# Optimization experiments

Hardware: AMD Instinct MI355X
Metric: run time of the kernel (lower is better)

Reference implementation:

```python
import jax, jax.numpy as jnp
import numpy as np

B, V, DIM, HEADS = 8192, 17, 192, 3
DKH = DIM // HEADS


def setup_inputs() -> dict:
    key = jax.random.key(0)
    ks = jax.random.split(key, 10)
    s = DIM ** -0.5
    return {
        "x": jax.random.normal(ks[0], (B, V, DIM), jnp.float32),
        "mask": jax.random.uniform(ks[1], (V, V), jnp.float32),
        "group_mask": jax.random.normal(ks[2], (B, HEADS, V, V), jnp.float32),
        "drop_mask": jax.random.bernoulli(ks[3], 0.5, (B, HEADS, V)).astype(jnp.float32),
        "qkv_w": jax.random.normal(ks[4], (3 * DIM, DIM), jnp.float32) * s,  # 1x1 conv == linear
        "qkv_b": jnp.zeros((3 * DIM,), jnp.float32),
        "attn_w": jax.random.normal(ks[5], (DIM, DIM), jnp.float32) * s,
        "attn_b": jnp.zeros((DIM,), jnp.float32),
        "key_rel": jax.random.normal(ks[6], (V * V - V, DKH), jnp.float32),
        "key_rel_diag": jax.random.normal(ks[7], (1, DKH), jnp.float32),
        "PA": jnp.ones((V, V), jnp.float32),
        "nn1_w": jax.random.normal(ks[8], (DIM, DIM), jnp.float32) * s,
        "nn1_b": jnp.zeros((DIM,), jnp.float32),
    }


def _forward(x, mask, group_mask, drop_mask, qkv_w, qkv_b, attn_w, attn_b,
             key_rel, key_rel_diag, PA, nn1_w, nn1_b):
    Bsz, Vn, C = x.shape
    Nh = HEADS
    dkh = C // Nh
    # 1x1 qkv conv over the channel axis (T=1 singleton time axis drops out)
    qkv = x @ qkv_w.T + qkv_b                      # (B, V, 3C)
    q, k, v = qkv[..., :C], qkv[..., C:2 * C], qkv[..., 2 * C:]

    def heads(t):
        return t.reshape(Bsz, Vn, Nh, dkh).transpose(0, 2, 1, 3)  # (B, Nh, V, dkh)

    q = heads(q) * (dkh ** -0.5)
    k = heads(k)
    v = heads(v)

    logits = jnp.einsum('bhid,bhjd->bhij', q, k)   # (B, Nh, V, V)
    logits = logits + (mask * PA)[None, None] + group_mask

    # relative position logits (rel_to_abs gather trick)
    rel = jnp.einsum('bhid,ijd->bhij', q, key_rel.reshape(Vn, Vn - 1, dkh))  # (B,Nh,V,V-1)
    diag = jnp.einsum('bhid,d->bhi', q, key_rel_diag[0])                     # (B,Nh,V)
    r = rel.reshape(Bsz, Nh, Vn - 1, Vn)           # reinterpret flat (V*(V-1)) as (V-1, V)
    r = jnp.concatenate([r, jnp.zeros((Bsz, Nh, 1, Vn), r.dtype)], axis=2)   # pad row -> (B,Nh,V,V)
    r = jnp.concatenate([diag[..., None], r], axis=3)                        # diag col -> (B,Nh,V,V+1)
    rel_logits = r.reshape(Bsz, Nh, Vn + 1, Vn)[:, :, :Vn, :]                # (B,Nh,V,V)

    w = jax.nn.softmax(logits + rel_logits, axis=-1)
    # stochastic column (key) mask + renormalize
    w = w * drop_mask[:, :, None, :]
    w = w / (w.sum(-1, keepdims=True) + 1e-8)

    out = jnp.einsum('bhij,bhjd->bhid', w, v)      # (B, Nh, V, dkh)
    out = out.transpose(0, 2, 1, 3).reshape(Bsz, Vn, C)  # combine heads (channel = h*dkh+d)
    out = out @ attn_w.T + attn_b                  # 1x1 attn_out conv
    out = out @ nn1_w.T + nn1_b                    # nn1 linear (dropout in eval -> identity)
    return out


def reference(x, mask, group_mask, drop_mask, qkv_w, qkv_b, attn_w, attn_b,
              key_rel, key_rel_diag, PA, nn1_w, nn1_b):
    return _forward(x, mask, group_mask, drop_mask, qkv_w, qkv_b, attn_w, attn_b,
                    key_rel, key_rel_diag, PA, nn1_w, nn1_b)
```

## Files before the change

kernel.cpp:

```cpp
#include <hip/hip_runtime.h>

typedef __attribute__((ext_vector_type(8))) short short8;
typedef __attribute__((ext_vector_type(4))) float f32x4;
typedef __attribute__((ext_vector_type(16))) float f32x16;
typedef unsigned short u16;
typedef unsigned int u32;

#define NB_TOT 8192
#define DIM 192

#define WN_OFF    0
#define WCN_OFF   221184
#define BC_OFF    294912
#define KRELF_OFF 295680
#define MPA_OFF   365312

#define XS_O  0
#define SF2_U16 3468
#define K_O   6944
#define V_O   13472
#define Q_O   22688
#define SMEM_U16 29264

__device__ __forceinline__ u16 f2b(float f) {
  u32 u = __float_as_uint(f);
  u32 r = u + 0x7FFFu + ((u >> 16) & 1u);
  return (u16)(r >> 16);
}

__device__ __forceinline__ int swzqk(int I) {
  return ((I & 7) << 3) ^ ((I & 8) << 1);
}

__device__ __forceinline__ void bar_lgkm() {
  asm volatile("s_waitcnt lgkmcnt(0)" ::: "memory");
  __builtin_amdgcn_s_barrier();
  asm volatile("" ::: "memory");
}

__global__ void prep_kernel(const float* __restrict__ qkv_w,
                            const float* __restrict__ attn_w,
                            const float* __restrict__ attn_b,
                            const float* __restrict__ nn1_w,
                            const float* __restrict__ nn1_b,
                            const float* __restrict__ key_rel,
                            const float* __restrict__ krd,
                            const float* __restrict__ mask,
                            const float* __restrict__ PA,
                            char* __restrict__ ws) {
  u16* wN    = (u16*)(ws + WN_OFF);
  u16* wcN   = (u16*)(ws + WCN_OFF);
  float* bc  = (float*)(ws + BC_OFF);
  u16* krelf = (u16*)(ws + KRELF_OFF);
  float* mpa = (float*)(ws + MPA_OFF);
  for (int idx = blockIdx.x * 256 + threadIdx.x; idx < 152289; idx += gridDim.x * 256) {
    if (idx < 110592) {
      wN[idx] = f2b(qkv_w[idx]);
    } else if (idx < 147456) {
      int t2 = idx - 110592; int n = t2 / 192, k = t2 - n * 192;
      float a = 0.f;
      for (int t = 0; t < 192; ++t) a = fmaf(nn1_w[n * 192 + t], attn_w[t * 192 + k], a);
      wcN[n * 192 + k] = f2b(a);
    } else if (idx < 147648) {
      int n = idx - 147456; float a = nn1_b[n];
      for (int t = 0; t < 192; ++t) a = fmaf(nn1_w[n * 192 + t], attn_b[t], a);
      bc[n] = a;
    } else if (idx < 152000) {
      int t = idx - 147648;
      int lane = t & 63, ks = (t >> 6) & 3, I = t >> 8;
      int J = lane & 31;
      int d0 = ks * 16 + (lane >> 5) * 8;
      u16 vals[8];
#pragma unroll
      for (int i = 0; i < 8; ++i) {
        float v = 0.f;
        if (J <= 16) {
          if (J == I) v = krd[d0 + i];
          else { int tt = 17 * I + J; int p = tt - tt / 18 - 1; v = key_rel[p * 64 + d0 + i]; }
        }
        vals[i] = f2b(v);
      }
      u32 w0 = vals[0] | ((u32)vals[1] << 16), w1 = vals[2] | ((u32)vals[3] << 16);
      u32 w2 = vals[4] | ((u32)vals[5] << 16), w3 = vals[6] | ((u32)vals[7] << 16);
      uint4 pk; pk.x = w0; pk.y = w1; pk.z = w2; pk.w = w3;
      *(uint4*)(krelf + (size_t)t * 8) = pk;
    } else {
      int i = idx - 152000; mpa[i] = mask[i] * PA[i];
    }
  }
}

__global__ __launch_bounds__(512, 4)
void fused_kernel(const float* __restrict__ x, const float* __restrict__ gm,
                  const float* __restrict__ drop, const float* __restrict__ qkv_b,
                  const u16* __restrict__ wN, const u16* __restrict__ wcN,
                  const float* __restrict__ bc, const u16* __restrict__ krelf,
                  const float* __restrict__ mpa, float* __restrict__ out) {
  __shared__ u16 smem[SMEM_U16];
  float* const Sf    = (float*)(smem + XS_O);
  float* const Sf2   = (float*)(smem + SF2_U16);
  u16*   const wbf   = smem + K_O;
  float* const dropl = (float*)(smem + K_O + 4080);

  const int tid = threadIdx.x;
  const int blk = blockIdx.x;
  const int lane = tid & 63;
  const int l31 = lane & 31;
  const int lh = lane >> 5;
  const int wv = tid >> 6;

  float drv = 0.f;
  if (tid < 102) drv = drop[(size_t)blk * 102 + tid];
  float gmr5[5] = {0.f, 0.f, 0.f, 0.f, 0.f};
  if (tid < 408) {
    int r = tid >> 2, sub = tid & 3;
    int bh = r / 17, I = r - bh * 17;
    const float* gmrow = gm + (size_t)blk * 1734 + bh * 289 + I * 17;
#pragma unroll
    for (int i = 0; i < 5; ++i) {
      int J = sub + 4 * i;
      if (J < 17) gmr5[i] = gmrow[J];
    }
  }

  const float* xb = x + (size_t)blk * 34 * 192;
  for (int idx = tid; idx < 1632; idx += 512) {
    int row = idx / 48, k4 = (idx - row * 48) * 4;
    float4 v = *(const float4*)(xb + row * 192 + k4);
    u16 p[4] = {f2b(v.x), f2b(v.y), f2b(v.z), f2b(v.w)};
    *(uint2*)(smem + XS_O + row * 200 + k4) = *(uint2*)p;
  }
  bar_lgkm();

  const int lrow = tid & 15, lg = (tid >> 4) & 3, kgrp = lg * 8;

  for (int Np = wv; Np < 18; Np += 8) {
    const int c0 = Np * 32;
    const int which = c0 / 192;
    const int hd0 = c0 - which * 192;
    const int h0 = hd0 >> 6,          h1 = (hd0 + 16) >> 6;
    const int d0 = (hd0 & 63) + lrow, d1 = ((hd0 + 16) & 63) + lrow;
    const u16* wB0 = wN + (size_t)(c0 + lrow) * 192;
    const u16* wB1 = wB0 + 16 * 192;
    short8 bfr0[6], bfr1[6];
#pragma unroll
    for (int kk = 0; kk < 6; ++kk) {
      bfr0[kk] = *(const short8*)(wB0 + kk * 32 + kgrp);
      bfr1[kk] = *(const short8*)(wB1 + kk * 32 + kgrp);
    }
    const float bias0 = qkv_b[c0 + lrow], bias1 = qkv_b[c0 + 16 + lrow];
    const float scale = which ? 1.0f : 0.125f;
#pragma unroll
    for (int m = 0; m < 3; ++m) {
      f32x4 acc0 = {}, acc1 = {};
#pragma unroll
      for (int kk = 0; kk < 6; ++kk) {
        short8 a = *(const short8*)(smem + XS_O + (m * 16 + lrow) * 200 + kk * 32 + kgrp);
        acc0 = __builtin_amdgcn_mfma_f32_16x16x32_bf16(a, bfr0[kk], acc0, 0, 0, 0);
        acc1 = __builtin_amdgcn_mfma_f32_16x16x32_bf16(a, bfr1[kk], acc1, 0, 0, 0);
      }
#pragma unroll
      for (int j = 0; j < 4; ++j) {
        int r = m * 16 + lg * 4 + j;
        if (r < 34) {
          int bi = r >= 17 ? 1 : 0, I = r - bi * 17;
          int slot = bi * 3 + h0, slot1 = bi * 3 + h1;
          u16 v0 = f2b((acc0[j] + bias0) * scale);
          u16 v1 = f2b((acc1[j] + bias1) * scale);
          if (which == 0) {
            smem[Q_O + slot  * 1096 + I * 64 + (d0 ^ swzqk(I))] = v0;
            smem[Q_O + slot1 * 1096 + I * 64 + (d1 ^ swzqk(I))] = v1;
          } else if (which == 1) {
            smem[K_O + slot  * 1088 + I * 64 + (d0 ^ swzqk(I))] = v0;
            smem[K_O + slot1 * 1088 + I * 64 + (d1 ^ swzqk(I))] = v1;
          } else {
            smem[V_O + slot  * 1536 + d0 * 24 + I] = v0;
            smem[V_O + slot1 * 1536 + d1 * 24 + I] = v1;
          }
        }
      }
    }
  }
  bar_lgkm();

  const int rowc = l31 < 16 ? l31 : 16;

  if (wv < 6) {
    int bh = wv;
    const u16* qb = smem + Q_O + bh * 1096;
    const u16* kb = smem + K_O + bh * 1088;
    const int swr = swzqk(rowc);
    f32x16 acc = {};
#pragma unroll
    for (int ks = 0; ks < 4; ++ks) {
      int off = (ks * 16 + lh * 8) ^ swr;
      short8 afr = *(const short8*)(qb + rowc * 64 + off);
      short8 bfr = *(const short8*)(kb + rowc * 64 + off);
      acc = __builtin_amdgcn_mfma_f32_32x32x16_bf16(afr, bfr, acc, 0, 0, 0);
    }
    if (l31 < 17) {
      float* Sb = Sf + bh * 289 + l31;
#pragma unroll
      for (int g = 0; g < 16; ++g) {
        int I = (g & 3) + 8 * (g >> 2) + 4 * lh;
        if (I < 17) Sb[I * 17] = acc[g];
      }
    }
  }
  for (int I = wv; I < 17; I += 8) {
    int bhA = l31 < 6 ? l31 : 5;
    const u16* qb = smem + Q_O + bhA * 1096 + I * 64;
    const int swz = swzqk(I);
    float mpav = (l31 < 17) ? mpa[I * 17 + l31] : 0.f;
    f32x16 acc = {};
#pragma unroll
    for (int ks = 0; ks < 4; ++ks) {
      short8 afr = *(const short8*)(qb + ((ks * 16 + lh * 8) ^ swz));
      short8 bfr = *(const short8*)(krelf + ((size_t)(I * 4 + ks) * 64 + lane) * 8);
      acc = __builtin_amdgcn_mfma_f32_32x32x16_bf16(afr, bfr, acc, 0, 0, 0);
    }
    if (l31 < 17) {
#pragma unroll
      for (int g = 0; g < 16; ++g) {
        int bh = (g & 3) + 8 * (g >> 2) + 4 * lh;
        if (bh < 6) Sf2[bh * 289 + I * 17 + l31] = acc[g] + mpav;
      }
    }
  }
  if (tid < 102) dropl[tid] = drv;
  bar_lgkm();

  if (tid < 408) {
    int r = tid >> 2, sub = tid & 3;
    int bh = r / 17, I = r - bh * 17;
    const float* Srow  = Sf  + bh * 289 + I * 17;
    const float* S2row = Sf2 + bh * 289 + I * 17;
    float lv[5];
    float mx = -3.4e38f;
#pragma unroll
    for (int i = 0; i < 5; ++i) {
      int J = sub + 4 * i;
      float v = -3.4e38f;
      if (J < 17) v = Srow[J] + S2row[J] + gmr5[i];
      lv[i] = v;
      mx = fmaxf(mx, v);
    }
    mx = fmaxf(mx, __shfl_xor(mx, 1, 4));
    mx = fmaxf(mx, __shfl_xor(mx, 2, 4));
    float s1 = 0.f;
#pragma unroll
    for (int i = 0; i < 5; ++i) {
      int J = sub + 4 * i;
      float e = 0.f;
      if (J < 17) e = __expf(lv[i] - mx);
      lv[i] = e; s1 += e;
    }
    s1 += __shfl_xor(s1, 1, 4);
    s1 += __shfl_xor(s1, 2, 4);
    float inv1 = 1.0f / s1, s2 = 0.f;
#pragma unroll
    for (int i = 0; i < 5; ++i) {
      int J = sub + 4 * i;
      float w2 = 0.f;
      if (J < 17) w2 = lv[i] * inv1 * dropl[bh * 17 + J];
      lv[i] = w2; s2 += w2;
    }
    s2 += __shfl_xor(s2, 1, 4);
    s2 += __shfl_xor(s2, 2, 4);
    float inv2 = 1.0f / (s2 + 1e-8f);
    u16* wr = wbf + r * 40;
    int swz = (I & 3) << 3;
#pragma unroll
    for (int i = 0; i < 8; ++i) {
      int J = sub + 4 * i;
      u16 val = 0;
      if (J < 17) val = f2b(lv[i] * inv2);
      wr[J ^ swz] = val;
    }
  }
  bar_lgkm();

  if (wv < 6) {
    int bh = wv;
    const u16* wb = wbf + (bh * 17 + rowc) * 40;
    int sw = (rowc & 3) << 3;
    short8 wa0 = *(const short8*)(wb + ((lh * 8) ^ sw));
    short8 wa1 = *(const short8*)(wb + ((lh * 8 + 16) ^ sw));
    int bi = bh >= 3 ? 1 : 0, h = bh - bi * 3;
    const u16* vb = smem + V_O + bh * 1536;
#pragma unroll
    for (int nt = 0; nt < 2; ++nt) {
      int d = nt * 32 + l31;
      short8 v0 = *(const short8*)(vb + d * 24 + lh * 8);
      f32x16 acc = {};
      acc = __builtin_amdgcn_mfma_f32_32x32x16_bf16(wa0, v0, acc, 0, 0, 0);
      short8 v1 = {};
      if (lh == 0) v1[0] = (short)vb[d * 24 + 16];
      acc = __builtin_amdgcn_mfma_f32_32x32x16_bf16(wa1, v1, acc, 0, 0, 0);
#pragma unroll
      for (int g = 0; g < 16; ++g) {
        int I = (g & 3) + 8 * (g >> 2) + 4 * lh;
        if (I < 17) smem[XS_O + (bi * 17 + I) * 200 + h * 64 + d] = f2b(acc[g]);
      }
    }
  }
  bar_lgkm();

  float* outb = out + (size_t)blk * 34 * 192;
  if (wv < 6) {
    const int nc0 = wv * 32 + lrow, nc1 = nc0 + 16;
    short8 bfr0[6], bfr1[6];
#pragma unroll
    for (int kk = 0; kk < 6; ++kk) {
      bfr0[kk] = *(const short8*)(wcN + (size_t)nc0 * 192 + kk * 32 + kgrp);
      bfr1[kk] = *(const short8*)(wcN + (size_t)nc1 * 192 + kk * 32 + kgrp);
    }
    const float bias0 = bc[nc0], bias1 = bc[nc1];
#pragma unroll
    for (int m = 0; m < 3; ++m) {
      f32x4 acc0 = {}, acc1 = {};
#pragma unroll
      for (int kk = 0; kk < 6; ++kk) {
        short8 a = *(const short8*)(smem + XS_O + (m * 16 + lrow) * 200 + kk * 32 + kgrp);
        acc0 = __builtin_amdgcn_mfma_f32_16x16x32_bf16(a, bfr0[kk], acc0, 0, 0, 0);
        acc1 = __builtin_amdgcn_mfma_f32_16x16x32_bf16(a, bfr1[kk], acc1, 0, 0, 0);
      }
#pragma unroll
      for (int j = 0; j < 4; ++j) {
        int r = m * 16 + lg * 4 + j;
        if (r < 34) {
          outb[(size_t)r * 192 + nc0] = acc0[j] + bias0;
          outb[(size_t)r * 192 + nc1] = acc1[j] + bias1;
        }
      }
    }
  }
}

extern "C" void kernel_launch(void* const* d_in, const int* in_sizes, int n_in,
                              void* d_out, int out_size, void* d_ws, size_t ws_size,
                              hipStream_t stream) {
  const float* x    = (const float*)d_in[0];
  const float* mask = (const float*)d_in[1];
  const float* gm   = (const float*)d_in[2];
  const float* drop = (const float*)d_in[3];
  const float* qkvw = (const float*)d_in[4];
  const float* qkvb = (const float*)d_in[5];
  const float* attw = (const float*)d_in[6];
  const float* attb = (const float*)d_in[7];
  const float* krel = (const float*)d_in[8];
  const float* krd  = (const float*)d_in[9];
  const float* PA   = (const float*)d_in[10];
  const float* nn1w = (const float*)d_in[11];
  const float* nn1b = (const float*)d_in[12];
  char* ws = (char*)d_ws;
  float* out = (float*)d_out;

  prep_kernel<<<600, 256, 0, stream>>>(qkvw, attw, attb, nn1w, nn1b, krel, krd, mask, PA, ws);

  const u16* wN    = (const u16*)(ws + WN_OFF);
  const u16* wcN   = (const u16*)(ws + WCN_OFF);
  const float* bc  = (const float*)(ws + BC_OFF);
  const u16* krelf = (const u16*)(ws + KRELF_OFF);
  const float* mpa = (const float*)(ws + MPA_OFF);

  fused_kernel<<<NB_TOT / 2, 512, 0, stream>>>(x, gm, drop, qkvb, wN, wcN, bc, krelf, mpa, out);
}
```

Measured before the change: 191.1 us.

## Split fused kernel into separate QKV GEMM and per-batch attention kernels

Adds a qkv_kernel that projects 64 rows of x at a time into a bf16 QKV buffer in the workspace, with the Q scale and bias already applied. It also adds an attn_kernel that runs one batch per 256-thread block, reads that buffer and performs attention plus the combined output projection. The aim is a larger, more efficient M-tile for the QKV GEMM and lower per-block shared memory, which should allow higher occupancy. The cost is an extra round trip through global memory for the roughly 160 MB bf16 QKV intermediate plus a second launch. The old fused kernel stays as a fallback when the workspace is too small.

```diff
diff --git a/kernel.cpp b/kernel.cpp
--- a/kernel.cpp
+++ b/kernel.cpp
@@ -14,13 +14,7 @@
 #define BC_OFF    294912
 #define KRELF_OFF 295680
 #define MPA_OFF   365312
-
-#define XS_O  0
-#define SF2_U16 3468
-#define K_O   6944
-#define V_O   13472
-#define Q_O   22688
-#define SMEM_U16 29264
+#define QKV_OFF   524288
 
 __device__ __forceinline__ u16 f2b(float f) {
   u32 u = __float_as_uint(f);
@@ -91,6 +85,265 @@
 }
 
 __global__ __launch_bounds__(512, 4)
+void qkv_kernel(const float* __restrict__ x, const u16* __restrict__ wN,
+                const float* __restrict__ qkv_b, u16* __restrict__ qkvo) {
+  __shared__ u16 xs[64 * 200];
+  const int tid = threadIdx.x;
+  const size_t R0 = (size_t)blockIdx.x * 64;
+  const float* xb = x + R0 * 192;
+  for (int idx = tid; idx < 3072; idx += 512) {
+    int row = idx / 48, k4 = (idx - row * 48) * 4;
+    float4 v = *(const float4*)(xb + row * 192 + k4);
+    u16 p[4] = {f2b(v.x), f2b(v.y), f2b(v.z), f2b(v.w)};
+    *(uint2*)(xs + row * 200 + k4) = *(uint2*)p;
+  }
+  bar_lgkm();
+  const int lrow = tid & 15, lg = (tid >> 4) & 3, kgrp = lg * 8;
+  const int wv = tid >> 6;
+  for (int Np = wv; Np < 18; Np += 8) {
+    const int c0 = Np * 32;
+    const int which = c0 / 192;
+    const u16* wB0 = wN + (size_t)(c0 + lrow) * 192;
+    const u16* wB1 = wB0 + 16 * 192;
+    short8 bfr0[6], bfr1[6];
+#pragma unroll
+    for (int kk = 0; kk < 6; ++kk) {
+      bfr0[kk] = *(const short8*)(wB0 + kk * 32 + kgrp);
+      bfr1[kk] = *(const short8*)(wB1 + kk * 32 + kgrp);
+    }
+    const float scale = which ? 1.0f : 0.125f;
+    const float bias0 = qkv_b[c0 + lrow], bias1 = qkv_b[c0 + 16 + lrow];
+#pragma unroll
+    for (int m = 0; m < 4; ++m) {
+      f32x4 acc0 = {}, acc1 = {};
+#pragma unroll
+      for (int kk = 0; kk < 6; ++kk) {
+        short8 a = *(const short8*)(xs + (m * 16 + lrow) * 200 + kk * 32 + kgrp);
+        acc0 = __builtin_amdgcn_mfma_f32_16x16x32_bf16(a, bfr0[kk], acc0, 0, 0, 0);
+        acc1 = __builtin_amdgcn_mfma_f32_16x16x32_bf16(a, bfr1[kk], acc1, 0, 0, 0);
+      }
+#pragma unroll
+      for (int j = 0; j < 4; ++j) {
+        int r = m * 16 + lg * 4 + j;
+        u16* dst = qkvo + (R0 + r) * 576;
+        dst[c0 + lrow]      = f2b((acc0[j] + bias0) * scale);
+        dst[c0 + 16 + lrow] = f2b((acc1[j] + bias1) * scale);
+      }
+    }
+  }
+}
+
+#define A_XS 0
+#define A_SF2 1734
+#define A_K  3472
+#define A_V  6736
+#define A_Q  10000
+#define A_SMEM 13288
+__global__ __launch_bounds__(256, 4)
+void attn_kernel(const u16* __restrict__ qkvo, const float* __restrict__ gm,
+                 const float* __restrict__ drop, const u16* __restrict__ wcN,
+                 const float* __restrict__ bc, const u16* __restrict__ krelf,
+                 const float* __restrict__ mpa, float* __restrict__ out) {
+  __shared__ u16 smem[A_SMEM];
+  float* const Sf    = (float*)(smem + A_XS);
+  float* const Sf2   = (float*)(smem + A_SF2);
+  u16*   const wbf   = smem + A_K;
+  float* const dropl = (float*)(smem + A_K + 1632);
+
+  const int tid = threadIdx.x;
+  const int blk = blockIdx.x;
+  const int lane = tid & 63;
+  const int l31 = lane & 31;
+  const int lh = lane >> 5;
+  const int wv = tid >> 6;
+
+  float drv = 0.f;
+  if (tid < 51) drv = drop[(size_t)blk * 51 + tid];
+  float gmr5[5] = {0.f, 0.f, 0.f, 0.f, 0.f};
+  if (tid < 204) {
+    int r = tid >> 2, sub = tid & 3;
+    int bh = r / 17, I = r - bh * 17;
+    const float* gmrow = gm + (size_t)blk * 867 + bh * 289 + I * 17;
+#pragma unroll
+    for (int i = 0; i < 5; ++i) {
+      int J = sub + 4 * i;
+      if (J < 17) gmr5[i] = gmrow[J];
+    }
+  }
+
+  const u16* qb0 = qkvo + (size_t)blk * 17 * 576;
+  for (int idx = tid; idx < 1224; idx += 256) {
+    int I = idx / 72, chunk = idx - I * 72;
+    int which = chunk / 24, r24 = chunk - which * 24;
+    int h = r24 >> 3, d0 = (r24 & 7) * 8;
+    short8 v = *(const short8*)(qb0 + I * 576 + which * 192 + h * 64 + d0);
+    if (which == 0)
+      *(short8*)(smem + A_Q + h * 1096 + I * 64 + (d0 ^ ((I & 7) << 3))) = v;
+    else if (which == 1)
+      *(short8*)(smem + A_K + h * 1088 + I * 64 + (d0 ^ ((I & 7) << 3))) = v;
+    else
+      *(short8*)(smem + A_V + h * 1088 + I * 64 + d0) = v;
+  }
+  bar_lgkm();
+
+  const int rowc = l31 < 16 ? l31 : 16;
+
+  if (wv < 3) {
+    int bh = wv;
+    const u16* qb = smem + A_Q + bh * 1096;
+    const u16* kb = smem + A_K + bh * 1088;
+    const int swr = (rowc & 7) << 3;
+    f32x16 acc = {};
+#pragma unroll
+    for (int ks = 0; ks < 4; ++ks) {
+      int off = (ks * 16 + lh * 8) ^ swr;
+      short8 afr = *(const short8*)(qb + rowc * 64 + off);
+      short8 bfr = *(const short8*)(kb + rowc * 64 + off);
+      acc = __builtin_amdgcn_mfma_f32_32x32x16_bf16(afr, bfr, acc, 0, 0, 0);
+    }
+    if (l31 < 17) {
+      float* Sb = Sf + bh * 289 + l31;
+#pragma unroll
+      for (int g = 0; g < 16; ++g) {
+        int I = (g & 3) + 8 * (g >> 2) + 4 * lh;
+        if (I < 17) Sb[I * 17] = acc[g];
+      }
+    }
+  }
+  for (int I = wv; I < 17; I += 4) {
+    int bhA = l31 < 3 ? l31 : 2;
+    const u16* qb = smem + A_Q + bhA * 1096 + I * 64;
+    const int swz = (I & 7) << 3;
+    float mpav = (l31 < 17) ? mpa[I * 17 + l31] : 0.f;
+    f32x16 acc = {};
+#pragma unroll
+    for (int ks = 0; ks < 4; ++ks) {
+      short8 afr = *(const short8*)(qb + ((ks * 16 + lh * 8) ^ swz));
+      short8 bfr = *(const short8*)(krelf + ((size_t)(I * 4 + ks) * 64 + lane) * 8);
+      acc = __builtin_amdgcn_mfma_f32_32x32x16_bf16(afr, bfr, acc, 0, 0, 0);
+    }
+    if (l31 < 17) {
+#pragma unroll
+      for (int g = 0; g < 16; ++g) {
+        int bh = (g & 3) + 8 * (g >> 2) + 4 * lh;
+        if (bh < 3) Sf2[bh * 289 + I * 17 + l31] = acc[g] + mpav;
+      }
+    }
+  }
+  if (tid < 51) dropl[tid] = drv;
+  bar_lgkm();
+
+  if (tid < 204) {
+    int r = tid >> 2, sub = tid & 3;
+    int bh = r / 17, I = r - bh * 17;
+    const float* Srow  = Sf  + bh * 289 + I * 17;
+    const float* S2row = Sf2 + bh * 289 + I * 17;
+    float lv[5];
+    float mx = -3.4e38f;
+#pragma unroll
+    for (int i = 0; i < 5; ++i) {
+      int J = sub + 4 * i;
+      float v = -3.4e38f;
+      if (J < 17) v = Srow[J] + S2row[J] + gmr5[i];
+      lv[i] = v;
+      mx = fmaxf(mx, v);
+    }
+    mx = fmaxf(mx, __shfl_xor(mx, 1, 4));
+    mx = fmaxf(mx, __shfl_xor(mx, 2, 4));
+    float s1 = 0.f;
+#pragma unroll
+    for (int i = 0; i < 5; ++i) {
+      int J = sub + 4 * i;
+      float e = 0.f;
+      if (J < 17) e = __expf(lv[i] - mx);
+      lv[i] = e; s1 += e;
+    }
+    s1 += __shfl_xor(s1, 1, 4);
+    s1 += __shfl_xor(s1, 2, 4);
+    float inv1 = 1.0f / s1, s2 = 0.f;
+#pragma unroll
+    for (int i = 0; i < 5; ++i) {
+      int J = sub + 4 * i;
+      float w2 = 0.f;
+      if (J < 17) w2 = lv[i] * inv1 * dropl[bh * 17 + J];
+      lv[i] = w2; s2 += w2;
+    }
+    s2 += __shfl_xor(s2, 1, 4);
+    s2 += __shfl_xor(s2, 2, 4);
+    float inv2 = 1.0f / (s2 + 1e-8f);
+    u16* wr = wbf + r * 32;
+    int swz = (I & 3) << 3;
+#pragma unroll
+    for (int i = 0; i < 8; ++i) {
+      int J = sub + 4 * i;
+      u16 val = 0;
+      if (J < 17) val = f2b(lv[i] * inv2);
+      wr[J ^ swz] = val;
+    }
+  }
+  bar_lgkm();
+
+  if (wv < 3) {
+    int bh = wv;
+    const u16* wb = wbf + (bh * 17 + rowc) * 32;
+    int sw = (rowc & 3) << 3;
+    short8 wa0 = *(const short8*)(wb + ((lh * 8) ^ sw));
+    short8 wa1 = *(const short8*)(wb + ((lh * 8 + 16) ^ sw));
+    const u16* vb = smem + A_V + bh * 1088;
+#pragma unroll
+    for (int nt = 0; nt < 2; ++nt) {
+      int d = nt * 32 + l31;
+      short8 v0;
+#pragma unroll
+      for (int i = 0; i < 8; ++i) v0[i] = (short)vb[(lh * 8 + i) * 64 + d];
+      f32x16 acc = {};
+      acc = __builtin_amdgcn_mfma_f32_32x32x16_bf16(wa0, v0, acc, 0, 0, 0);
+      short8 v1 = {};
+      if (lh == 0) v1[0] = (short)vb[16 * 64 + d];
+      acc = __builtin_amdgcn_mfma_f32_32x32x16_bf16(wa1, v1, acc, 0, 0, 0);
+#pragma unroll
+      for (int g = 0; g < 16; ++g) {
+        int I = (g & 3) + 8 * (g >> 2) + 4 * lh;
+        if (I < 17) smem[A_XS + I * 200 + bh * 64 + d] = f2b(acc[g]);
+      }
+    }
+  }
+  bar_lgkm();
+
+  float* outb = out + (size_t)blk * 17 * 192;
+  const int lrow = tid & 15, lg = (tid >> 4) & 3, kgrp = lg * 8;
+  for (int n = wv; n < 12; n += 4) {
+    const int nc = n * 16 + lrow;
+    short8 bfr[6];
+#pragma unroll
+    for (int kk = 0; kk < 6; ++kk)
+      bfr[kk] = *(const short8*)(wcN + (size_t)nc * 192 + kk * 32 + kgrp);
+    const float bias = bc[nc];
+#pragma unroll
+    for (int m = 0; m < 2; ++m) {
+      f32x4 acc = {};
+#pragma unroll
+      for (int kk = 0; kk < 6; ++kk) {
+        short8 a = *(const short8*)(smem + A_XS + (m * 16 + lrow) * 200 + kk * 32 + kgrp);
+        acc = __builtin_amdgcn_mfma_f32_16x16x32_bf16(a, bfr[kk], acc, 0, 0, 0);
+      }
+#pragma unroll
+      for (int j = 0; j < 4; ++j) {
+        int r = m * 16 + lg * 4 + j;
+        if (r < 17) outb[(size_t)r * 192 + nc] = acc[j] + bias;
+      }
+    }
+  }
+}
+
+#define XS_O  0
+#define SF2_U16 3468
+#define K_O   6944
+#define V_O   13472
+#define Q_O   22688
+#define SMEM_U16 29264
+
+__global__ __launch_bounds__(512, 4)
 void fused_kernel(const float* __restrict__ x, const float* __restrict__ gm,
                   const float* __restrict__ drop, const float* __restrict__ qkv_b,
                   const u16* __restrict__ wN, const u16* __restrict__ wcN,
@@ -364,5 +617,12 @@
   const u16* krelf = (const u16*)(ws + KRELF_OFF);
   const float* mpa = (const float*)(ws + MPA_OFF);
 
-  fused_kernel<<<NB_TOT / 2, 512, 0, stream>>>(x, gm, drop, qkvb, wN, wcN, bc, krelf, mpa, out);
-}
+  const size_t need = (size_t)QKV_OFF + (size_t)139264 * 576 * 2;
+  if (ws_size >= need) {
+    u16* qkvo = (u16*)(ws + QKV_OFF);
+    qkv_kernel<<<2176, 512, 0, stream>>>(x, wN, qkvb, qkvo);
+    attn_kernel<<<NB_TOT, 256, 0, stream>>>(qkvo, gm, drop, wcN, bc, krelf, mpa, out);
+  } else {
+    fused_kernel<<<NB_TOT / 2, 512, 0, stream>>>(x, gm, drop, qkvb, wN, wcN, bc, krelf, mpa, out);
+  }
+}
```

After: 292.6 us. +53.1%, slower.
